# Kernel optimization log

Measured on AMD Instinct MI355X. Metric: run time of the kernel, lower is better.

Reference implementation:

```python
import jax, jax.numpy as jnp
import numpy as np

DEPTH, B, H, E = 4, 4096, 1024, 1024  # embedDim == h so all layers stack


def setup_inputs() -> dict:
    key = jax.random.key(0)
    k1, k2, k3, k4 = jax.random.split(key, 4)
    x = jax.random.normal(k1, (B, E), dtype=jnp.float32)
    s_h = jax.random.normal(k2, (DEPTH, B, H), dtype=jnp.float32)
    s_c = jax.random.normal(k3, (DEPTH, B, H), dtype=jnp.float32)
    # Linear(embedDim + h, 4h) per layer; stored as [in, out] (transposed torch layout)
    W = jax.random.normal(k4, (DEPTH, E + H, 4 * H), dtype=jnp.float32) * 0.02
    b = jnp.zeros((DEPTH, 4 * H), dtype=jnp.float32)
    return {"x": x, "s_h": s_h, "s_c": s_c, "W": W, "b": b}


def _lstm_layer(out, layer_params):
    hh, c, Wl, bl = layer_params
    xh = jnp.concatenate([out, hh], axis=1)          # [B, E+H]
    z = xh @ Wl + bl                                  # [B, 4H]
    i, f, o, g = jnp.split(z, 4, axis=1)              # torch.split(Wx, h, 1) order: i,f,o,g
    i = jax.nn.sigmoid(i)
    f = jax.nn.sigmoid(f)
    o = jax.nn.sigmoid(o)
    g = jnp.tanh(g)
    # trainable=False -> no dropout on g
    c_new = c * f + g * i
    h_new = jnp.tanh(c_new) * o
    return h_new, (h_new, c_new)


def reference(x, s_h, s_c, W, b):
    # scan over depth: layer l consumes previous layer's output as its input
    out, (h_new, c_new) = jax.lax.scan(_lstm_layer, x, (s_h, s_c, W, b))
    return out, h_new, c_new
```

## Files before the change

### kernel.cpp

```cpp
#include <hip/hip_runtime.h>
#include <hip/hip_bf16.h>
#include <stdint.h>

#define DEPTH 4
#define Bb 4096
#define Hh 1024
#define Ee 1024
#define Kd 2048
#define Ng 4096
#define NT (Kd / 64)

typedef __attribute__((ext_vector_type(8))) short short8;
typedef __attribute__((ext_vector_type(4))) float floatx4;
typedef __attribute__((ext_vector_type(4))) float f32x4;

__device__ __forceinline__ float fast_sigmoid(float x) {
  return 1.0f / (1.0f + __expf(-x));
}
__device__ __forceinline__ float fast_tanh(float x) {
  float t = __expf(-2.0f * fabsf(x));
  return copysignf((1.0f - t) / (1.0f + t), x);
}

__device__ __forceinline__ void gload_lds16(const void* g, void* l) {
  __builtin_amdgcn_global_load_lds(
      (const __attribute__((address_space(1))) void*)(uintptr_t)g,
      (__attribute__((address_space(3))) void*)(uint32_t)(uintptr_t)l,
      16, 0, 0);
}

__global__ __launch_bounds__(256) void transpose_w_kernel(
    const float* __restrict__ W, __hip_bfloat16* __restrict__ Wt) {
  __shared__ __attribute__((aligned(16))) float ldsT[64 * 132];
  const int l = blockIdx.z;
  const int k0 = blockIdx.x * 128;
  const int n0 = blockIdx.y * 64;
  const float* Wl = W + (size_t)l * Kd * Ng + (size_t)k0 * Ng + n0;
  __hip_bfloat16* Wtl = Wt + (size_t)l * Ng * Kd;
  const int tid = threadIdx.x;

#pragma unroll
  for (int i = 0; i < 8; i++) {
    const int flat = tid + 256 * i;
    const int k = flat >> 4;
    const int c4 = (flat & 15) * 4;
    const f32x4 v = *(const f32x4*)(Wl + (size_t)k * Ng + c4);
    const int grp = k >> 3;
    const int klo = k & 7;
#pragma unroll
    for (int j = 0; j < 4; j++) {
      const int n = c4 + j;
      ldsT[n * 132 + ((grp ^ ((n >> 2) & 3)) << 3) + klo] = v[j];
    }
  }
  __syncthreads();

#pragma unroll
  for (int i = 0; i < 4; i++) {
    const int c = tid + 256 * i;
    const int n = c >> 4;
    const int kc = c & 15;
    const int g = kc ^ ((n >> 2) & 3);
    const float* src = &ldsT[n * 132 + (g << 3)];
    const f32x4 u0 = *(const f32x4*)src;
    const f32x4 u1 = *(const f32x4*)(src + 4);
    union {
      __hip_bfloat16 h[8];
      short8 s;
    } p;
    p.h[0] = __float2bfloat16(u0.x);
    p.h[1] = __float2bfloat16(u0.y);
    p.h[2] = __float2bfloat16(u0.z);
    p.h[3] = __float2bfloat16(u0.w);
    p.h[4] = __float2bfloat16(u1.x);
    p.h[5] = __float2bfloat16(u1.y);
    p.h[6] = __float2bfloat16(u1.z);
    p.h[7] = __float2bfloat16(u1.w);
    *(short8*)&Wtl[(size_t)(n0 + n) * Kd + k0 + kc * 8] = p.s;
  }
}

__global__ __launch_bounds__(256) void prefill_xh_kernel(
    const float* __restrict__ x, const float* __restrict__ s_h,
    __hip_bfloat16* __restrict__ xh) {
  const int idx = blockIdx.x * blockDim.x + threadIdx.x;
  const int XN = Bb * Ee / 4;
  const int TOTAL = XN + DEPTH * Bb * Hh / 4;
  if (idx >= TOTAL) return;
  const float* srcp;
  __hip_bfloat16* dst;
  if (idx < XN) {
    const int b = idx >> 8;
    const int j4 = idx & 255;
    srcp = x + (size_t)idx * 4;
    dst = xh + (size_t)b * Kd + j4 * 4;
  } else {
    const int e4 = idx - XN;
    const int l = e4 >> 20;
    const int r = e4 & 0xFFFFF;
    const int b = r >> 8;
    const int j4 = r & 255;
    srcp = s_h + (size_t)e4 * 4;
    dst = xh + (size_t)l * Bb * Kd + (size_t)b * Kd + Ee + j4 * 4;
  }
  f32x4 v = *(const f32x4*)srcp;
  union {
    __hip_bfloat16 h[4];
    unsigned long long u;
  } p;
  p.h[0] = __float2bfloat16(v.x);
  p.h[1] = __float2bfloat16(v.y);
  p.h[2] = __float2bfloat16(v.z);
  p.h[3] = __float2bfloat16(v.w);
  *(unsigned long long*)dst = p.u;
}

__global__ __launch_bounds__(512, 2) void lstm_layer_kernel(
    const __hip_bfloat16* __restrict__ A, const __hip_bfloat16* __restrict__ Wt,
    const float* __restrict__ bias, const float* __restrict__ c_in,
    float* __restrict__ out_h, float* __restrict__ out_c,
    float* __restrict__ out_final, __hip_bfloat16* __restrict__ xh_next) {
  __shared__ __attribute__((aligned(16))) __hip_bfloat16 sm[4 * 256 * 64];

  const int tid = threadIdx.x;
  const int lane = tid & 63;
  const int wave = tid >> 6;
  const int wm = wave >> 2;
  const int wn = wave & 3;
  const int m0 = blockIdx.y * 256;
  const int j0 = blockIdx.x * 64;

  const int r0 = tid >> 3;
  const int p = tid & 7;
  const int q = p ^ (r0 & 7);
  const __hip_bfloat16* aS = A + (size_t)(m0 + r0) * Kd + q * 8;
  const __hip_bfloat16* bS = Wt + (size_t)(j0 + r0) * Kd + q * 8;

#define STAGEA(h, kt, buf)                                          \
  do {                                                              \
    __hip_bfloat16* _d = sm + (buf) * 16384 + (h) * 8192 + tid * 8; \
    gload_lds16(aS + (size_t)((h) * 128) * Kd + (kt) * 64, _d);     \
    gload_lds16(aS + (size_t)((h) * 128 + 64) * Kd + (kt) * 64,     \
                _d + 4096);                                         \
  } while (0)
#define STAGEB(h, kt, buf)                                                  \
  do {                                                                      \
    __hip_bfloat16* _d = sm + 32768 + (buf) * 16384 + (h) * 8192 + tid * 8; \
    gload_lds16(bS + (size_t)((h) * 2) * 1024 * Kd + (kt) * 64, _d);        \
    gload_lds16(bS + (size_t)((h) * 2 + 1) * 1024 * Kd + (kt) * 64,         \
                _d + 4096);                                                 \
  } while (0)

  const int qk = lane >> 4;
  const int lm = lane & 15;
  const int pc0 = qk ^ (lm & 7);
  const int pc1 = (4 + qk) ^ (lm & 7);
  const int aBase = (wm * 128 + lm) * 64;
  const int bBase = (wn * 16 + lm) * 64;

  floatx4 acc[8][4];
#pragma unroll
  for (int mi = 0; mi < 8; mi++)
#pragma unroll
    for (int g = 0; g < 4; g++) acc[mi][g] = floatx4{0.f, 0.f, 0.f, 0.f};

  STAGEA(0, 0, 0);
  STAGEA(1, 0, 0);
  STAGEB(0, 0, 0);
  STAGEB(1, 0, 0);
  STAGEA(0, 1, 1);
  STAGEA(1, 1, 1);
  STAGEB(0, 1, 1);
  asm volatile("s_waitcnt vmcnt(6)" ::: "memory");
  __builtin_amdgcn_sched_barrier(0);
  __builtin_amdgcn_s_barrier();

  for (int t = 0; t < NT; ++t) {
    const int cur = t & 1;
    const __hip_bfloat16* As_c = sm + cur * 16384;
    const __hip_bfloat16* Bs_c = sm + 32768 + cur * 16384;

    short8 af[8][2];
    short8 bfg[4][2];

#pragma unroll
    for (int mi = 0; mi < 4; mi++) {
      af[mi][0] = *(const short8*)&As_c[aBase + mi * 1024 + pc0 * 8];
      af[mi][1] = *(const short8*)&As_c[aBase + mi * 1024 + pc1 * 8];
    }
#pragma unroll
    for (int g = 0; g < 2; g++) {
      bfg[g][0] = *(const short8*)&Bs_c[bBase + g * 4096 + pc0 * 8];
      bfg[g][1] = *(const short8*)&Bs_c[bBase + g * 4096 + pc1 * 8];
    }
    if (t + 1 < NT) STAGEB(1, t + 1, cur ^ 1);
#pragma unroll
    for (int mi = 4; mi < 8; mi++) {
      af[mi][0] = *(const short8*)&As_c[aBase + mi * 1024 + pc0 * 8];
      af[mi][1] = *(const short8*)&As_c[aBase + mi * 1024 + pc1 * 8];
    }
#pragma unroll
    for (int g = 2; g < 4; g++) {
      bfg[g][0] = *(const short8*)&Bs_c[bBase + g * 4096 + pc0 * 8];
      bfg[g][1] = *(const short8*)&Bs_c[bBase + g * 4096 + pc1 * 8];
    }

    __builtin_amdgcn_s_setprio(1);
#pragma unroll
    for (int mi = 0; mi < 8; mi++)
#pragma unroll
      for (int g = 0; g < 2; g++) {
        acc[mi][g] = __builtin_amdgcn_mfma_f32_16x16x32_bf16(
            af[mi][0], bfg[g][0], acc[mi][g], 0, 0, 0);
        acc[mi][g] = __builtin_amdgcn_mfma_f32_16x16x32_bf16(
            af[mi][1], bfg[g][1], acc[mi][g], 0, 0, 0);
      }
    __builtin_amdgcn_s_setprio(0);

    asm volatile("s_waitcnt lgkmcnt(0)" ::: "memory");
    __builtin_amdgcn_sched_barrier(0);
    __builtin_amdgcn_s_barrier();

    if (t + 2 < NT) {
      STAGEA(0, t + 2, cur);
      STAGEA(1, t + 2, cur);
      STAGEB(0, t + 2, cur);
    }

    __builtin_amdgcn_s_setprio(1);
#pragma unroll
    for (int mi = 0; mi < 8; mi++)
#pragma unroll
      for (int g = 2; g < 4; g++) {
        acc[mi][g] = __builtin_amdgcn_mfma_f32_16x16x32_bf16(
            af[mi][0], bfg[g][0], acc[mi][g], 0, 0, 0);
        acc[mi][g] = __builtin_amdgcn_mfma_f32_16x16x32_bf16(
            af[mi][1], bfg[g][1], acc[mi][g], 0, 0, 0);
      }
    __builtin_amdgcn_s_setprio(0);

    if (t < NT - 2)
      asm volatile("s_waitcnt vmcnt(6)" ::: "memory");
    else
      asm volatile("s_waitcnt vmcnt(0)" ::: "memory");
    __builtin_amdgcn_sched_barrier(0);
    __builtin_amdgcn_s_barrier();
  }

  const int j = j0 + wn * 16 + lm;
  const float bi = bias[j];
  const float bf_ = bias[Hh + j];
  const float bo = bias[2 * Hh + j];
  const float bg = bias[3 * Hh + j];
#pragma unroll
  for (int mi = 0; mi < 8; mi++) {
    const int row0 = m0 + wm * 128 + mi * 16 + qk * 4;
#pragma unroll
    for (int r = 0; r < 4; r++) {
      const int row = row0 + r;
      const float zi = acc[mi][0][r] + bi;
      const float zf = acc[mi][1][r] + bf_;
      const float zo = acc[mi][2][r] + bo;
      const float zg = acc[mi][3][r] + bg;
      const float ig = fast_sigmoid(zi);
      const float fg = fast_sigmoid(zf);
      const float og = fast_sigmoid(zo);
      const float gg = fast_tanh(zg);
      const float c = c_in[(size_t)row * Hh + j];
      const float cn = fmaf(c, fg, gg * ig);
      const float hn = fast_tanh(cn) * og;
      out_h[(size_t)row * Hh + j] = hn;
      out_c[(size_t)row * Hh + j] = cn;
      if (xh_next) xh_next[(size_t)row * Kd + j] = __float2bfloat16(hn);
      if (out_final) out_final[(size_t)row * Hh + j] = hn;
    }
  }
#undef STAGEA
#undef STAGEB
}

extern "C" void kernel_launch(void* const* d_in, const int* in_sizes, int n_in,
                              void* d_out, int out_size, void* d_ws,
                              size_t ws_size, hipStream_t stream) {
  const float* x = (const float*)d_in[0];
  const float* s_h = (const float*)d_in[1];
  const float* s_c = (const float*)d_in[2];
  const float* W = (const float*)d_in[3];
  const float* bias = (const float*)d_in[4];
  float* out = (float*)d_out;

  __hip_bfloat16* Wt = (__hip_bfloat16*)d_ws;
  __hip_bfloat16* xh =
      (__hip_bfloat16*)((char*)d_ws + (size_t)DEPTH * Ng * Kd * 2);

  transpose_w_kernel<<<dim3(Kd / 128, Ng / 64, DEPTH), 256, 0, stream>>>(W, Wt);
  prefill_xh_kernel<<<(Bb * Ee / 4 + DEPTH * Bb * Hh / 4) / 256, 256, 0,
                      stream>>>(x, s_h, xh);

  float* out_h = out + (size_t)Bb * Ee;
  float* out_c = out_h + (size_t)DEPTH * Bb * Hh;
  for (int l = 0; l < DEPTH; l++) {
    lstm_layer_kernel<<<dim3(Hh / 64, Bb / 256), 512, 0, stream>>>(
        xh + (size_t)l * Bb * Kd, Wt + (size_t)l * Ng * Kd,
        bias + (size_t)l * Ng, s_c + (size_t)l * Bb * Hh,
        out_h + (size_t)l * Bb * Hh, out_c + (size_t)l * Bb * Hh,
        (l == DEPTH - 1) ? out : nullptr,
        (l < DEPTH - 1) ? xh + (size_t)(l + 1) * Bb * Kd : nullptr);
  }
}
```

Before: 654.1 us.

## Prefetch next-tile MFMA fragments into registers and use a single barrier per iteration

Restructures the bf16 GEMM main loop so the A and B fragments for the next K-tile are loaded from LDS into registers during the current tile's MFMAs. Splits the MFMAs into four quadrants interleaved with partial lgkmcnt waits, and moves all staging of the tile two steps ahead to after one barrier per iteration. The goal is to hide LDS read latency and cut barrier overhead. The trade-off is a full vmcnt(0) wait each iteration, which may expose global-load latency, plus higher register pressure.

Result: no change. 653.6 us (-0.1%).

```diff
diff --git a/kernel.cpp b/kernel.cpp
--- a/kernel.cpp
+++ b/kernel.cpp
@@ -164,6 +164,23 @@
 #pragma unroll
     for (int g = 0; g < 4; g++) acc[mi][g] = floatx4{0.f, 0.f, 0.f, 0.f};
 
+  short8 af0[4][2];
+  short8 af1[4][2];
+  short8 b01[2][2];
+  short8 b23[2][2];
+
+#define QUAD16(MB, GB, AF, BF)                                              \
+  do {                                                                      \
+    _Pragma("unroll") for (int mi = 0; mi < 4; mi++) {                      \
+      _Pragma("unroll") for (int g = 0; g < 2; g++) {                       \
+        acc[(MB) + mi][(GB) + g] = __builtin_amdgcn_mfma_f32_16x16x32_bf16( \
+            AF[mi][0], BF[g][0], acc[(MB) + mi][(GB) + g], 0, 0, 0);        \
+        acc[(MB) + mi][(GB) + g] = __builtin_amdgcn_mfma_f32_16x16x32_bf16( \
+            AF[mi][1], BF[g][1], acc[(MB) + mi][(GB) + g], 0, 0, 0);        \
+      }                                                                     \
+    }                                                                       \
+  } while (0)
+
   STAGEA(0, 0, 0);
   STAGEA(1, 0, 0);
   STAGEB(0, 0, 0);
@@ -171,80 +188,87 @@
   STAGEA(0, 1, 1);
   STAGEA(1, 1, 1);
   STAGEB(0, 1, 1);
-  asm volatile("s_waitcnt vmcnt(6)" ::: "memory");
+  STAGEB(1, 1, 1);
+  asm volatile("s_waitcnt vmcnt(8)" ::: "memory");
   __builtin_amdgcn_sched_barrier(0);
   __builtin_amdgcn_s_barrier();
+  {
+    const __hip_bfloat16* As0 = sm;
+    const __hip_bfloat16* Bs0 = sm + 32768;
+#pragma unroll
+    for (int mi = 0; mi < 4; mi++) {
+      af0[mi][0] = *(const short8*)&As0[aBase + mi * 1024 + pc0 * 8];
+      af0[mi][1] = *(const short8*)&As0[aBase + mi * 1024 + pc1 * 8];
+    }
+#pragma unroll
+    for (int g = 0; g < 2; g++) {
+      b23[g][0] = *(const short8*)&Bs0[bBase + (g + 2) * 4096 + pc0 * 8];
+      b23[g][1] = *(const short8*)&Bs0[bBase + (g + 2) * 4096 + pc1 * 8];
+    }
+  }
 
   for (int t = 0; t < NT; ++t) {
     const int cur = t & 1;
     const __hip_bfloat16* As_c = sm + cur * 16384;
     const __hip_bfloat16* Bs_c = sm + 32768 + cur * 16384;
-
-    short8 af[8][2];
-    short8 bfg[4][2];
+    const __hip_bfloat16* As_n = sm + (cur ^ 1) * 16384;
+    const __hip_bfloat16* Bs_n = sm + 32768 + (cur ^ 1) * 16384;
+
+#pragma unroll
+    for (int g = 0; g < 2; g++) {
+      b01[g][0] = *(const short8*)&Bs_c[bBase + g * 4096 + pc0 * 8];
+      b01[g][1] = *(const short8*)&Bs_c[bBase + g * 4096 + pc1 * 8];
+    }
+    asm volatile("s_waitcnt lgkmcnt(4)" ::: "memory");
+    __builtin_amdgcn_sched_barrier(0);
+    __builtin_amdgcn_s_setprio(1);
+    QUAD16(0, 2, af0, b23);
+    __builtin_amdgcn_s_setprio(0);
 
 #pragma unroll
     for (int mi = 0; mi < 4; mi++) {
-      af[mi][0] = *(const short8*)&As_c[aBase + mi * 1024 + pc0 * 8];
-      af[mi][1] = *(const short8*)&As_c[aBase + mi * 1024 + pc1 * 8];
-    }
-#pragma unroll
-    for (int g = 0; g < 2; g++) {
-      bfg[g][0] = *(const short8*)&Bs_c[bBase + g * 4096 + pc0 * 8];
-      bfg[g][1] = *(const short8*)&Bs_c[bBase + g * 4096 + pc1 * 8];
-    }
-    if (t + 1 < NT) STAGEB(1, t + 1, cur ^ 1);
-#pragma unroll
-    for (int mi = 4; mi < 8; mi++) {
-      af[mi][0] = *(const short8*)&As_c[aBase + mi * 1024 + pc0 * 8];
-      af[mi][1] = *(const short8*)&As_c[aBase + mi * 1024 + pc1 * 8];
-    }
-#pragma unroll
-    for (int g = 2; g < 4; g++) {
-      bfg[g][0] = *(const short8*)&Bs_c[bBase + g * 4096 + pc0 * 8];
-      bfg[g][1] = *(const short8*)&Bs_c[bBase + g * 4096 + pc1 * 8];
-    }
-
+      af1[mi][0] = *(const short8*)&As_c[aBase + (mi + 4) * 1024 + pc0 * 8];
+      af1[mi][1] = *(const short8*)&As_c[aBase + (mi + 4) * 1024 + pc1 * 8];
+    }
+    asm volatile("s_waitcnt lgkmcnt(8)" ::: "memory");
+    __builtin_amdgcn_sched_barrier(0);
     __builtin_amdgcn_s_setprio(1);
-#pragma unroll
-    for (int mi = 0; mi < 8; mi++)
-#pragma unroll
-      for (int g = 0; g < 2; g++) {
-        acc[mi][g] = __builtin_amdgcn_mfma_f32_16x16x32_bf16(
-            af[mi][0], bfg[g][0], acc[mi][g], 0, 0, 0);
-        acc[mi][g] = __builtin_amdgcn_mfma_f32_16x16x32_bf16(
-            af[mi][1], bfg[g][1], acc[mi][g], 0, 0, 0);
-      }
+    QUAD16(0, 0, af0, b01);
     __builtin_amdgcn_s_setprio(0);
 
     asm volatile("s_waitcnt lgkmcnt(0)" ::: "memory");
+    asm volatile("s_waitcnt vmcnt(0)" ::: "memory");
     __builtin_amdgcn_sched_barrier(0);
     __builtin_amdgcn_s_barrier();
 
+    if (t + 1 < NT) {
+#pragma unroll
+      for (int mi = 0; mi < 4; mi++) {
+        af0[mi][0] = *(const short8*)&As_n[aBase + mi * 1024 + pc0 * 8];
+        af0[mi][1] = *(const short8*)&As_n[aBase + mi * 1024 + pc1 * 8];
+      }
+    }
     if (t + 2 < NT) {
       STAGEA(0, t + 2, cur);
       STAGEA(1, t + 2, cur);
       STAGEB(0, t + 2, cur);
+      STAGEB(1, t + 2, cur);
     }
 
     __builtin_amdgcn_s_setprio(1);
-#pragma unroll
-    for (int mi = 0; mi < 8; mi++)
-#pragma unroll
-      for (int g = 2; g < 4; g++) {
-        acc[mi][g] = __builtin_amdgcn_mfma_f32_16x16x32_bf16(
-            af[mi][0], bfg[g][0], acc[mi][g], 0, 0, 0);
-        acc[mi][g] = __builtin_amdgcn_mfma_f32_16x16x32_bf16(
-            af[mi][1], bfg[g][1], acc[mi][g], 0, 0, 0);
+    QUAD16(4, 0, af1, b01);
+    __builtin_amdgcn_s_setprio(0);
+
+    __builtin_amdgcn_s_setprio(1);
+    QUAD16(4, 2, af1, b23);
+    __builtin_amdgcn_s_setprio(0);
+    if (t + 1 < NT) {
+#pragma unroll
+      for (int g = 0; g < 2; g++) {
+        b23[g][0] = *(const short8*)&Bs_n[bBase + (g + 2) * 4096 + pc0 * 8];
+        b23[g][1] = *(const short8*)&Bs_n[bBase + (g + 2) * 4096 + pc1 * 8];
       }
-    __builtin_amdgcn_s_setprio(0);
-
-    if (t < NT - 2)
-      asm volatile("s_waitcnt vmcnt(6)" ::: "memory");
-    else
-      asm volatile("s_waitcnt vmcnt(0)" ::: "memory");
-    __builtin_amdgcn_sched_barrier(0);
-    __builtin_amdgcn_s_barrier();
+    }
   }
 
   const int j = j0 + wn * 16 + lm;
@@ -277,6 +301,7 @@
   }
 #undef STAGEA
 #undef STAGEB
+#undef QUAD16
 }
 
 extern "C" void kernel_launch(void* const* d_in, const int* in_sizes, int n_in,
```
